# Performance work log

Measured on AMD Instinct MI355X. Metric: run time of the kernel, lower is better.

Reference implementation:

```python
import jax, jax.numpy as jnp
import numpy as np

MIN_NORM = 1e-15
PROJ_EPS = 4e-3  # float32 boundary eps used by hgcn PoincareBall.proj
C = 1.0          # curvature for every layer
N, E, D = 10000, 320000, 256


def _norm(x):
    return jnp.maximum(jnp.linalg.norm(x, axis=-1, keepdims=True), MIN_NORM)


def artanh(x):
    return jnp.arctanh(jnp.clip(x, -1 + 1e-7, 1 - 1e-7))


def proj(x, c):
    norm = _norm(x)
    maxnorm = (1.0 - PROJ_EPS) / jnp.sqrt(c)
    return jnp.where(norm > maxnorm, x / norm * maxnorm, x)


def expmap0(u, c):
    sqrt_c = jnp.sqrt(c)
    u_norm = _norm(u)
    return jnp.tanh(sqrt_c * u_norm) * u / (sqrt_c * u_norm)


def logmap0(p, c):
    sqrt_c = jnp.sqrt(c)
    p_norm = _norm(p)
    return artanh(sqrt_c * p_norm) * p / (sqrt_c * p_norm)


def mobius_add(x, y, c):
    x2 = jnp.sum(x * x, -1, keepdims=True)
    y2 = jnp.sum(y * y, -1, keepdims=True)
    xy = jnp.sum(x * y, -1, keepdims=True)
    num = (1 + 2 * c * xy + c * y2) * x + (1 - c * x2) * y
    denom = 1 + 2 * c * xy + c * c * x2 * y2
    return num / jnp.maximum(denom, MIN_NORM)


def mobius_matvec(m, x, c):
    sqrt_c = jnp.sqrt(c)
    x_norm = _norm(x)
    mx = x @ m.T
    mx_norm = _norm(mx)
    res = jnp.tanh(mx_norm / x_norm * artanh(sqrt_c * x_norm)) * mx / (mx_norm * sqrt_c)
    zero_row = jnp.all(mx == 0, axis=-1, keepdims=True)
    return jnp.where(zero_row, jnp.zeros_like(res), res)


def hgc_layer(h, W, b, edge_weight, edge_src, edge_dst, c):
    # HypLinear (dropout=0, eval mode)
    res = proj(mobius_matvec(W, h, c), c)
    hyp_bias = proj(expmap0(b[None, :], c), c)
    h = proj(mobius_add(res, hyp_bias, c), c)
    # HypAgg: tangent-space neighborhood aggregation (spmm over edge list)
    xt = logmap0(h, c)                                  # [N, D]
    msgs = edge_weight[:, None] * xt[edge_src]          # [E, D] irregular gather
    agg = jax.ops.segment_sum(msgs, edge_dst, num_segments=N)
    h = proj(expmap0(agg, c), c)
    # HypAct: relu in tangent space, map back with c_out
    xt = jax.nn.relu(logmap0(h, c))
    return proj(expmap0(xt, c), c)


def setup_inputs() -> dict:
    key = jax.random.key(0)
    ks = jax.random.split(key, 8)
    x = jax.random.normal(ks[0], (N, D), dtype=jnp.float32)
    edge_src = jax.random.randint(ks[1], (E,), 0, N)
    edge_dst = jax.random.randint(ks[2], (E,), 0, N)
    # normalized-adjacency-like positive weights (~1/deg scale)
    edge_weight = jax.random.uniform(ks[3], (E,), dtype=jnp.float32) / 32.0
    s = 1.0 / np.sqrt(D)
    W1 = jax.random.normal(ks[4], (D, D), dtype=jnp.float32) * s
    b1 = jnp.zeros((D,), dtype=jnp.float32)
    W2 = jax.random.normal(ks[5], (D, D), dtype=jnp.float32) * s
    b2 = jnp.zeros((D,), dtype=jnp.float32)
    return {"x": x, "W1": W1, "b1": b1, "W2": W2, "b2": b2,
            "edge_weight": edge_weight, "edge_src": edge_src, "edge_dst": edge_dst}


def reference(x, W1, b1, W2, b2, edge_weight, edge_src, edge_dst):
    # old=True path: map Euclidean features onto the Poincare ball first
    h = proj(expmap0(x, C), C)
    h = hgc_layer(h, W1, b1, edge_weight, edge_src, edge_dst, C)
    h = hgc_layer(h, W2, b2, edge_weight, edge_src, edge_dst, C)
    return h
```

## Files before the change

### kernel.cpp

```cpp
#include <hip/hip_runtime.h>
#include <hip/hip_fp16.h>

#define DIM 256
#define MAXNORM 0.996f
#define MINN 1e-15f
#define CLIPV 0.9999999f

typedef __attribute__((ext_vector_type(8))) short bf16x8;
typedef __attribute__((ext_vector_type(4))) float f32x4;

__device__ __forceinline__ unsigned short f2bf(float f) {
    unsigned int u = __float_as_uint(f);
    u += 0x7fffu + ((u >> 16) & 1u);
    return (unsigned short)(u >> 16);
}
__device__ __forceinline__ float h2f(unsigned short h) {
    return __half2float(__ushort_as_half(h));
}
__device__ __forceinline__ unsigned short f2h(float f) {
    return __half_as_ushort(__float2half(f));
}
__device__ __forceinline__ float wsum(float v) {
    v += __shfl_xor(v, 32);
    v += __shfl_xor(v, 16);
    v += __shfl_xor(v, 8);
    v += __shfl_xor(v, 4);
    v += __shfl_xor(v, 2);
    v += __shfl_xor(v, 1);
    return v;
}

__global__ void k_setup(const float* __restrict__ x, unsigned short* __restrict__ h_bf,
                        float* __restrict__ hnorm2, int nrows,
                        int* __restrict__ csr_off, int nOff,
                        const float* __restrict__ W1, const float* __restrict__ W2,
                        unsigned short* __restrict__ w_bf, int nPerW, int eB) {
    int bid = blockIdx.x;
    if (bid < eB) {
        int gid = bid * 256 + threadIdx.x;
        int row = gid >> 6, lane = gid & 63;
        if (row >= nrows) return;
        size_t base = (size_t)row * DIM + lane * 4;
        float4 v = *(const float4*)(x + base);
        float ss = wsum(v.x * v.x + v.y * v.y + v.z * v.z + v.w * v.w);
        float n = fmaxf(sqrtf(ss), MINN);
        float tn = tanhf(n);
        float hn = (tn > MAXNORM) ? MAXNORM : tn;
        float s = hn / n;
        ushort4 ob;
        ob.x = f2bf(v.x * s); ob.y = f2bf(v.y * s);
        ob.z = f2bf(v.z * s); ob.w = f2bf(v.w * s);
        *(ushort4*)(h_bf + base) = ob;
        if (lane == 0) hnorm2[row] = hn * hn;
    } else if (bid < eB + 64) {
        int i = (bid - eB) * 256 + threadIdx.x;
        int stride = 64 * 256;
        for (; i < nOff; i += stride) csr_off[i] = 0;
    } else {
        int i = (bid - eB - 64) * 256 + threadIdx.x;
        int stride = 128 * 256;
        for (; i < 2 * nPerW; i += stride)
            w_bf[i] = f2bf(i < nPerW ? W1[i] : W2[i - nPerW]);
    }
}

__global__ void k_hist(const int* __restrict__ dst, int* __restrict__ off, int nE, int nrows) {
    int e = blockIdx.x * blockDim.x + threadIdx.x;
    if (e >= nE) return;
    int d = dst[e];
    if (d >= 0 && d < nrows) atomicAdd(&off[d + 1], 1);
}

__global__ void k_scan(int* __restrict__ a, int* __restrict__ cursor, int n) {
    __shared__ int wsums[16];
    int t = threadIdx.x;
    int chunk = (n + 1023) / 1024;
    int lo = t * chunk, hi = min(lo + chunk, n);
    int sum = 0;
    for (int i = lo; i < hi; ++i) sum += a[i];
    int lane = t & 63, wid = t >> 6;
    int v = sum;
    for (int o = 1; o < 64; o <<= 1) {
        int u = __shfl_up(v, o);
        if (lane >= o) v += u;
    }
    if (lane == 63) wsums[wid] = v;
    __syncthreads();
    if (t == 0) {
        int c = 0;
        for (int i = 0; i < 16; ++i) { int x = wsums[i]; wsums[i] = c; c += x; }
    }
    __syncthreads();
    int excl = v - sum + wsums[wid];
    int c = excl;
    for (int i = lo; i < hi; ++i) {
        c += a[i];
        a[i] = c;
        if (i < n - 1) cursor[i] = c;
    }
}

__global__ void k_fill(const int* __restrict__ esrc, const int* __restrict__ edst,
                       const float* __restrict__ ew, int* __restrict__ cursor,
                       int2* __restrict__ csr_pack, int nE, int nrows) {
    int e = blockIdx.x * blockDim.x + threadIdx.x;
    if (e >= nE) return;
    int d = edst[e];
    if (d < 0 || d >= nrows) return;
    int pos = atomicAdd(&cursor[d], 1);
    csr_pack[pos] = make_int2(esrc[e], __float_as_int(ew[e]));
}

__global__ void k_gemm_mfma(const unsigned short* __restrict__ Abf,
                            const unsigned short* __restrict__ Wbf,
                            unsigned short* __restrict__ C16, int M) {
    int wave = threadIdx.x >> 6;
    int lane = threadIdx.x & 63;
    int r = lane & 15, oct = lane >> 4;
    int i0 = blockIdx.y * 64 + wave * 16;
    int j0 = blockIdx.x * 16;
    int arow = i0 + r;
    bool av = arow < M;
    const unsigned short* ap = Abf + (size_t)arow * DIM + oct * 8;
    const unsigned short* bp = Wbf + (size_t)(j0 + r) * DIM + oct * 8;
    const bf16x8 zf = {0, 0, 0, 0, 0, 0, 0, 0};
    f32x4 acc = {0.f, 0.f, 0.f, 0.f};
#pragma unroll
    for (int k0 = 0; k0 < 256; k0 += 32) {
        bf16x8 a = av ? *(const bf16x8*)(ap + k0) : zf;
        bf16x8 b = *(const bf16x8*)(bp + k0);
        acc = __builtin_amdgcn_mfma_f32_16x16x32_bf16(a, b, acc, 0, 0, 0);
    }
#pragma unroll
    for (int q = 0; q < 4; ++q) {
        int row = i0 + oct * 4 + q;
        if (row < M) C16[(size_t)row * DIM + j0 + r] = f2h(acc[q]);
    }
}

__global__ void k_post(const unsigned short* __restrict__ MX16, const float* __restrict__ hnorm2,
                       const float* __restrict__ b, unsigned short* __restrict__ XT, int nrows) {
    int gid = blockIdx.x * blockDim.x + threadIdx.x;
    int row = gid >> 6, lane = gid & 63;
    if (row >= nrows) return;
    size_t base = (size_t)row * DIM + lane * 4;
    ushort4 mu = *(const ushort4*)(MX16 + base);
    float m0 = h2f(mu.x), m1 = h2f(mu.y), m2 = h2f(mu.z), m3 = h2f(mu.w);
    float4 bv = *(const float4*)(b + lane * 4);
    float bs = wsum(bv.x * bv.x + bv.y * bv.y + bv.z * bv.z + bv.w * bv.w);
    float bn = fmaxf(sqrtf(bs), MINN);
    float btn = tanhf(bn);
    float bhn = (btn > MAXNORM) ? MAXNORM : btn;
    float bscale = bhn / bn;
    float e0 = bv.x * bscale, e1 = bv.y * bscale, e2 = bv.z * bscale, e3 = bv.w * bscale;
    float y2 = bhn * bhn;

    float sm = wsum(m0 * m0 + m1 * m1 + m2 * m2 + m3 * m3);
    float sxy = wsum(m0 * e0 + m1 * e1 + m2 * e2 + m3 * e3);
    float sh = hnorm2[row];
    float xn = fmaxf(sqrtf(sh), MINN);
    float at = atanhf(fminf(xn, CLIPV));
    float mn = fmaxf(sqrtf(sm), MINN);
    float t = tanhf(mn / xn * at);
    float alpha = t / mn;
    float resn = t;
    if (t > MAXNORM) { alpha = MAXNORM / mn; resn = MAXNORM; }
    float x2 = resn * resn;
    float xy = alpha * sxy;
    float Aa = 1.f + 2.f * xy + y2;
    float Bb = 1.f - x2;
    float den = fmaxf(1.f + 2.f * xy + x2 * y2, MINN);
    float s_m = Aa * alpha / den;
    float s_b = Bb / den;
    float hn2 = (Aa * Aa * x2 + 2.f * Aa * Bb * xy + Bb * Bb * y2) / (den * den);
    float hn = fmaxf(sqrtf(fmaxf(hn2, 0.f)), MINN);
    if (hn > MAXNORM) { float f = MAXNORM / hn; s_m *= f; s_b *= f; hn = MAXNORM; }
    float lt = atanhf(fminf(hn, CLIPV)) / hn;
    s_m *= lt; s_b *= lt;
    ushort4 o;
    o.x = f2h(s_m * m0 + s_b * e0);
    o.y = f2h(s_m * m1 + s_b * e1);
    o.z = f2h(s_m * m2 + s_b * e2);
    o.w = f2h(s_m * m3 + s_b * e3);
    *(ushort4*)(XT + base) = o;
}

__global__ void k_agg_finish(const unsigned short* __restrict__ XT, const int* __restrict__ off,
                             const int2* __restrict__ cpk,
                             float* __restrict__ OUT, unsigned short* __restrict__ OUT_bf,
                             float* __restrict__ hnorm2, int nrows) {
    int gid = blockIdx.x * blockDim.x + threadIdx.x;
    int row = gid >> 6, lane = gid & 63;
    if (row >= nrows) return;
    int p0 = off[row], p1 = off[row + 1];
    float a0 = 0.f, a1 = 0.f, a2 = 0.f, a3 = 0.f;
    int p = p0;
    for (; p + 7 < p1; p += 8) {
        ushort4 v[8];
        float w[8];
#pragma unroll
        for (int u = 0; u < 8; ++u) {
            int2 pk = cpk[p + u];
            w[u] = __int_as_float(pk.y);
            v[u] = *(const ushort4*)(XT + (size_t)pk.x * DIM + lane * 4);
        }
#pragma unroll
        for (int u = 0; u < 8; ++u) {
            a0 = fmaf(w[u], h2f(v[u].x), a0);
            a1 = fmaf(w[u], h2f(v[u].y), a1);
            a2 = fmaf(w[u], h2f(v[u].z), a2);
            a3 = fmaf(w[u], h2f(v[u].w), a3);
        }
    }
    for (; p < p1; ++p) {
        int2 pk = cpk[p];
        float w = __int_as_float(pk.y);
        ushort4 v = *(const ushort4*)(XT + (size_t)pk.x * DIM + lane * 4);
        a0 = fmaf(w, h2f(v.x), a0); a1 = fmaf(w, h2f(v.y), a1);
        a2 = fmaf(w, h2f(v.z), a2); a3 = fmaf(w, h2f(v.w), a3);
    }
    float ss = wsum(a0 * a0 + a1 * a1 + a2 * a2 + a3 * a3);
    float n = fmaxf(sqrtf(ss), MINN);
    float tn = tanhf(n);
    float hn = (tn > MAXNORM) ? MAXNORM : tn;
    float s1 = hn / n;
    float lt = atanhf(fminf(hn, CLIPV)) / fmaxf(hn, MINN);
    float s2 = lt * s1;
    float x0 = fmaxf(s2 * a0, 0.f), x1 = fmaxf(s2 * a1, 0.f);
    float x2 = fmaxf(s2 * a2, 0.f), x3 = fmaxf(s2 * a3, 0.f);
    float ss2 = wsum(x0 * x0 + x1 * x1 + x2 * x2 + x3 * x3);
    float n2 = fmaxf(sqrtf(ss2), MINN);
    float tn2 = tanhf(n2);
    float hn2c = (tn2 > MAXNORM) ? MAXNORM : tn2;
    float s3 = hn2c / n2;
    float o0 = s3 * x0, o1 = s3 * x1, o2 = s3 * x2, o3 = s3 * x3;
    size_t base = (size_t)row * DIM + lane * 4;
    if (OUT_bf) {
        ushort4 ob;
        ob.x = f2bf(o0); ob.y = f2bf(o1); ob.z = f2bf(o2); ob.w = f2bf(o3);
        *(ushort4*)(OUT_bf + base) = ob;
        if (lane == 0) hnorm2[row] = hn2c * hn2c;
    } else {
        *(float4*)(OUT + base) = make_float4(o0, o1, o2, o3);
    }
}

static inline size_t align256(size_t x) { return (x + 255) & ~(size_t)255; }

extern "C" void kernel_launch(void* const* d_in, const int* in_sizes, int n_in,
                              void* d_out, int out_size, void* d_ws, size_t ws_size,
                              hipStream_t stream) {
    const float* x  = (const float*)d_in[0];
    const float* W1 = (const float*)d_in[1];
    const float* b1 = (const float*)d_in[2];
    const float* W2 = (const float*)d_in[3];
    const float* b2 = (const float*)d_in[4];
    const float* ew = (const float*)d_in[5];
    const int* esrc = (const int*)d_in[6];
    const int* edst = (const int*)d_in[7];
    const int nE = in_sizes[5];
    const int M  = in_sizes[0] / DIM;

    size_t S = (size_t)M * DIM;
    char* base = (char*)d_ws;
    size_t o = 0;
    int2* csr_pack = (int2*)(base + o);          o = align256(o + (size_t)nE * 8);
    int* csr_off   = (int*)(base + o);           o = align256(o + (size_t)(M + 1) * 4);
    int* cursor    = (int*)(base + o);           o = align256(o + (size_t)M * 4);
    float* hnorm2  = (float*)(base + o);         o = align256(o + (size_t)(M + 64) * 4);
    unsigned short* xt   = (unsigned short*)(base + o);  o = align256(o + S * 2);
    unsigned short* h_bf = (unsigned short*)(base + o);  o = align256(o + S * 2);
    unsigned short* mx16 = (unsigned short*)(base + o);  o = align256(o + S * 2);
    unsigned short* w_bf = (unsigned short*)(base + o);  o = align256(o + (size_t)2 * DIM * DIM * 2);

    int rowBlocks = (M + 3) / 4;
    dim3 gemmGrid(DIM / 16, (M + 63) / 64);
    int edgeBlocks = (nE + 255) / 256;

    k_setup<<<rowBlocks + 64 + 128, 256, 0, stream>>>(
        x, h_bf, hnorm2, M, csr_off, M + 1, W1, W2, w_bf, DIM * DIM, rowBlocks);

    k_hist<<<edgeBlocks, 256, 0, stream>>>(edst, csr_off, nE, M);
    k_scan<<<1, 1024, 0, stream>>>(csr_off, cursor, M + 1);
    k_fill<<<edgeBlocks, 256, 0, stream>>>(esrc, edst, ew, cursor, csr_pack, nE, M);

    for (int layer = 0; layer < 2; ++layer) {
        const float* b = (layer == 0) ? b1 : b2;
        const unsigned short* Wb = w_bf + (size_t)layer * DIM * DIM;
        k_gemm_mfma<<<gemmGrid, 256, 0, stream>>>(h_bf, Wb, mx16, M);
        k_post<<<rowBlocks, 256, 0, stream>>>(mx16, hnorm2, b, xt, M);
        k_agg_finish<<<rowBlocks, 256, 0, stream>>>(
            xt, csr_off, csr_pack,
            (layer == 0) ? (float*)nullptr : (float*)d_out,
            (layer == 0) ? h_bf : (unsigned short*)nullptr,
            hnorm2, M);
    }
}
```

Before: 244.0 us.

## Fuse MFMA GEMM with hyperbolic post-processing into one row-stripe kernel

Replaces the separate GEMM and post-processing kernels with one kernel. Each 512-thread block computes a full 16-row stripe of all 256 output columns, reduces row norms and bias dot products through shared memory, and writes the tangent-space result directly. This removes the fp16 intermediate buffer round trip and one launch per layer. In exchange the stripe layout has fewer blocks, and every block re-reads the whole weight matrix.

Measured after the change: 246.3 us. About the same (+1.0%).

```diff
diff --git a/kernel.cpp b/kernel.cpp
--- a/kernel.cpp
+++ b/kernel.cpp
@@ -27,6 +27,13 @@
     v += __shfl_xor(v, 4);
     v += __shfl_xor(v, 2);
     v += __shfl_xor(v, 1);
+    return v;
+}
+__device__ __forceinline__ float wsum16(float v) {
+    v += __shfl_xor(v, 1);
+    v += __shfl_xor(v, 2);
+    v += __shfl_xor(v, 4);
+    v += __shfl_xor(v, 8);
     return v;
 }
 
@@ -111,78 +118,103 @@
     csr_pack[pos] = make_int2(esrc[e], __float_as_int(ew[e]));
 }
 
-__global__ void k_gemm_mfma(const unsigned short* __restrict__ Abf,
+__global__ void k_gemm_post(const unsigned short* __restrict__ Abf,
                             const unsigned short* __restrict__ Wbf,
-                            unsigned short* __restrict__ C16, int M) {
+                            const float* __restrict__ hnorm2,
+                            const float* __restrict__ b,
+                            unsigned short* __restrict__ XT, int M) {
+    __shared__ float sm_part[8][16];
+    __shared__ float sxy_part[8][16];
     int wave = threadIdx.x >> 6;
     int lane = threadIdx.x & 63;
     int r = lane & 15, oct = lane >> 4;
-    int i0 = blockIdx.y * 64 + wave * 16;
-    int j0 = blockIdx.x * 16;
+    int i0 = blockIdx.x * 16;
     int arow = i0 + r;
     bool av = arow < M;
     const unsigned short* ap = Abf + (size_t)arow * DIM + oct * 8;
-    const unsigned short* bp = Wbf + (size_t)(j0 + r) * DIM + oct * 8;
     const bf16x8 zf = {0, 0, 0, 0, 0, 0, 0, 0};
-    f32x4 acc = {0.f, 0.f, 0.f, 0.f};
-#pragma unroll
-    for (int k0 = 0; k0 < 256; k0 += 32) {
-        bf16x8 a = av ? *(const bf16x8*)(ap + k0) : zf;
-        bf16x8 b = *(const bf16x8*)(bp + k0);
-        acc = __builtin_amdgcn_mfma_f32_16x16x32_bf16(a, b, acc, 0, 0, 0);
-    }
-#pragma unroll
-    for (int q = 0; q < 4; ++q) {
-        int row = i0 + oct * 4 + q;
-        if (row < M) C16[(size_t)row * DIM + j0 + r] = f2h(acc[q]);
-    }
-}
-
-__global__ void k_post(const unsigned short* __restrict__ MX16, const float* __restrict__ hnorm2,
-                       const float* __restrict__ b, unsigned short* __restrict__ XT, int nrows) {
-    int gid = blockIdx.x * blockDim.x + threadIdx.x;
-    int row = gid >> 6, lane = gid & 63;
-    if (row >= nrows) return;
-    size_t base = (size_t)row * DIM + lane * 4;
-    ushort4 mu = *(const ushort4*)(MX16 + base);
-    float m0 = h2f(mu.x), m1 = h2f(mu.y), m2 = h2f(mu.z), m3 = h2f(mu.w);
-    float4 bv = *(const float4*)(b + lane * 4);
-    float bs = wsum(bv.x * bv.x + bv.y * bv.y + bv.z * bv.z + bv.w * bv.w);
-    float bn = fmaxf(sqrtf(bs), MINN);
+    bf16x8 afrag[8];
+#pragma unroll
+    for (int kc = 0; kc < 8; ++kc)
+        afrag[kc] = av ? *(const bf16x8*)(ap + kc * 32) : zf;
+
+    int jbase = wave * 32;
+    f32x4 acc[2];
+#pragma unroll
+    for (int t = 0; t < 2; ++t) {
+        acc[t] = (f32x4){0.f, 0.f, 0.f, 0.f};
+        const unsigned short* bp = Wbf + (size_t)(jbase + t * 16 + r) * DIM + oct * 8;
+#pragma unroll
+        for (int kc = 0; kc < 8; ++kc) {
+            bf16x8 bb = *(const bf16x8*)(bp + kc * 32);
+            acc[t] = __builtin_amdgcn_mfma_f32_16x16x32_bf16(afrag[kc], bb, acc[t], 0, 0, 0);
+        }
+    }
+
+    float4 bq = *(const float4*)(b + lane * 4);
+    float bss = wsum(bq.x * bq.x + bq.y * bq.y + bq.z * bq.z + bq.w * bq.w);
+    float bn = fmaxf(sqrtf(bss), MINN);
     float btn = tanhf(bn);
     float bhn = (btn > MAXNORM) ? MAXNORM : btn;
     float bscale = bhn / bn;
-    float e0 = bv.x * bscale, e1 = bv.y * bscale, e2 = bv.z * bscale, e3 = bv.w * bscale;
     float y2 = bhn * bhn;
-
-    float sm = wsum(m0 * m0 + m1 * m1 + m2 * m2 + m3 * m3);
-    float sxy = wsum(m0 * e0 + m1 * e1 + m2 * e2 + m3 * e3);
-    float sh = hnorm2[row];
-    float xn = fmaxf(sqrtf(sh), MINN);
-    float at = atanhf(fminf(xn, CLIPV));
-    float mn = fmaxf(sqrtf(sm), MINN);
-    float t = tanhf(mn / xn * at);
-    float alpha = t / mn;
-    float resn = t;
-    if (t > MAXNORM) { alpha = MAXNORM / mn; resn = MAXNORM; }
-    float x2 = resn * resn;
-    float xy = alpha * sxy;
-    float Aa = 1.f + 2.f * xy + y2;
-    float Bb = 1.f - x2;
-    float den = fmaxf(1.f + 2.f * xy + x2 * y2, MINN);
-    float s_m = Aa * alpha / den;
-    float s_b = Bb / den;
-    float hn2 = (Aa * Aa * x2 + 2.f * Aa * Bb * xy + Bb * Bb * y2) / (den * den);
-    float hn = fmaxf(sqrtf(fmaxf(hn2, 0.f)), MINN);
-    if (hn > MAXNORM) { float f = MAXNORM / hn; s_m *= f; s_b *= f; hn = MAXNORM; }
-    float lt = atanhf(fminf(hn, CLIPV)) / hn;
-    s_m *= lt; s_b *= lt;
-    ushort4 o;
-    o.x = f2h(s_m * m0 + s_b * e0);
-    o.y = f2h(s_m * m1 + s_b * e1);
-    o.z = f2h(s_m * m2 + s_b * e2);
-    o.w = f2h(s_m * m3 + s_b * e3);
-    *(ushort4*)(XT + base) = o;
+    float bv[2];
+#pragma unroll
+    for (int t = 0; t < 2; ++t) bv[t] = b[jbase + t * 16 + r];
+
+#pragma unroll
+    for (int q = 0; q < 4; ++q) {
+        float smv = 0.f, dotv = 0.f;
+#pragma unroll
+        for (int t = 0; t < 2; ++t) {
+            float m = acc[t][q];
+            smv = fmaf(m, m, smv);
+            dotv = fmaf(m, bv[t], dotv);
+        }
+        smv = wsum16(smv);
+        dotv = wsum16(dotv);
+        if (r == 0) {
+            sm_part[wave][oct * 4 + q] = smv;
+            sxy_part[wave][oct * 4 + q] = dotv;
+        }
+    }
+    __syncthreads();
+
+#pragma unroll
+    for (int q = 0; q < 4; ++q) {
+        int lr = oct * 4 + q;
+        float sm = 0.f, sxyr = 0.f;
+#pragma unroll
+        for (int w = 0; w < 8; ++w) { sm += sm_part[w][lr]; sxyr += sxy_part[w][lr]; }
+        float sxy = sxyr * bscale;
+        int R = i0 + lr;
+        float sh = (R < M) ? hnorm2[R] : 1.0f;
+        float xn = fmaxf(sqrtf(sh), MINN);
+        float at = atanhf(fminf(xn, CLIPV));
+        float mn = fmaxf(sqrtf(sm), MINN);
+        float t = tanhf(mn / xn * at);
+        float alpha = t / mn;
+        float resn = t;
+        if (t > MAXNORM) { alpha = MAXNORM / mn; resn = MAXNORM; }
+        float x2 = resn * resn;
+        float xy = alpha * sxy;
+        float Aa = 1.f + 2.f * xy + y2;
+        float Bb = 1.f - x2;
+        float den = fmaxf(1.f + 2.f * xy + x2 * y2, MINN);
+        float s_m = Aa * alpha / den;
+        float s_b = Bb / den;
+        float hn2 = (Aa * Aa * x2 + 2.f * Aa * Bb * xy + Bb * Bb * y2) / (den * den);
+        float hn = fmaxf(sqrtf(fmaxf(hn2, 0.f)), MINN);
+        if (hn > MAXNORM) { float f = MAXNORM / hn; s_m *= f; s_b *= f; hn = MAXNORM; }
+        float lt = atanhf(fminf(hn, CLIPV)) / hn;
+        s_m *= lt; s_b *= lt;
+        if (R < M) {
+            unsigned short* op = XT + (size_t)R * DIM + jbase + r;
+#pragma unroll
+            for (int t2 = 0; t2 < 2; ++t2)
+                op[t2 * 16] = f2h(fmaf(s_m, acc[t2][q], s_b * (bscale * bv[t2])));
+        }
+    }
 }
 
 __global__ void k_agg_finish(const unsigned short* __restrict__ XT, const int* __restrict__ off,
@@ -270,11 +302,10 @@
     float* hnorm2  = (float*)(base + o);         o = align256(o + (size_t)(M + 64) * 4);
     unsigned short* xt   = (unsigned short*)(base + o);  o = align256(o + S * 2);
     unsigned short* h_bf = (unsigned short*)(base + o);  o = align256(o + S * 2);
-    unsigned short* mx16 = (unsigned short*)(base + o);  o = align256(o + S * 2);
     unsigned short* w_bf = (unsigned short*)(base + o);  o = align256(o + (size_t)2 * DIM * DIM * 2);
 
     int rowBlocks = (M + 3) / 4;
-    dim3 gemmGrid(DIM / 16, (M + 63) / 64);
+    int stripeBlocks = (M + 15) / 16;
     int edgeBlocks = (nE + 255) / 256;
 
     k_setup<<<rowBlocks + 64 + 128, 256, 0, stream>>>(
@@ -287,8 +318,7 @@
     for (int layer = 0; layer < 2; ++layer) {
         const float* b = (layer == 0) ? b1 : b2;
         const unsigned short* Wb = w_bf + (size_t)layer * DIM * DIM;
-        k_gemm_mfma<<<gemmGrid, 256, 0, stream>>>(h_bf, Wb, mx16, M);
-        k_post<<<rowBlocks, 256, 0, stream>>>(mx16, hnorm2, b, xt, M);
+        k_gemm_post<<<stripeBlocks, 512, 0, stream>>>(h_bf, Wb, hnorm2, b, xt, M);
         k_agg_finish<<<rowBlocks, 256, 0, stream>>>(
             xt, csr_off, csr_pack,
             (layer == 0) ? (float*)nullptr : (float*)d_out,
```
